# Optimization experiments

Measured on AMD Instinct MI355X. Metric: run time of the kernel, lower is better.

The kernel has to match this reference:

```python
import jax, jax.numpy as jnp
import numpy as np

N_EMBED = 384
NUM_HEADS = 6
HEAD_SIZE = N_EMBED // NUM_HEADS  # 64
B, T = 8, 2048


def setup_inputs() -> dict:
    key = jax.random.key(0)
    ks = jax.random.split(key, 8)
    s = 1.0 / np.sqrt(N_EMBED)
    query = jax.random.normal(ks[0], (B, T, N_EMBED), dtype=jnp.float32)
    key_t = jax.random.normal(ks[1], (B, T, N_EMBED), dtype=jnp.float32)
    value = jax.random.normal(ks[2], (B, T, N_EMBED), dtype=jnp.float32)
    # causal-style mask, broadcastable over (B, H)
    mask = jnp.tril(jnp.ones((T, T), dtype=jnp.int32))[None, None]
    Wk = jax.random.normal(ks[3], (N_EMBED, N_EMBED), dtype=jnp.float32) * s
    Wq = jax.random.normal(ks[4], (N_EMBED, N_EMBED), dtype=jnp.float32) * s
    Wv = jax.random.normal(ks[5], (N_EMBED, N_EMBED), dtype=jnp.float32) * s
    Wproj = jax.random.normal(ks[6], (N_EMBED, N_EMBED), dtype=jnp.float32) * s
    bproj = jnp.zeros((N_EMBED,), dtype=jnp.float32)
    return {"query": query, "key": key_t, "value": value, "mask": mask,
            "Wk": Wk, "Wq": Wq, "Wv": Wv, "Wproj": Wproj, "bproj": bproj}


def _split_heads(x):
    b, t, c = x.shape
    return x.reshape(b, t, NUM_HEADS, c // NUM_HEADS).transpose(0, 2, 1, 3)  # [B,H,T,D]


def reference(query, key, value, mask, Wk, Wq, Wv, Wproj, bproj):
    b, t, c = query.shape
    # NOTE: source swaps names: k = key_proj(query), q = query_proj(key)
    k = _split_heads(query @ Wk.T)
    q = _split_heads(key @ Wq.T)
    v = _split_heads(value @ Wv.T)
    # scale by full C (not head_size), as in the source
    wei = jnp.einsum("bhqd,bhkd->bhqk", q, k) * (c ** -0.5)
    # masked_fill with 0 BEFORE softmax (faithful to source)
    wei = jnp.where(mask == 0, jnp.float32(0.0), wei)
    wei = jax.nn.softmax(wei, axis=-1)
    out = jnp.einsum("bhqk,bhkd->bhqd", wei, v)
    out = out.transpose(0, 2, 1, 3).reshape(b, t, c)
    out = out @ Wproj.T + bproj  # dropout is identity at inference
    return out
```

## Files before the change

### kernel.cpp

```cpp
#include <hip/hip_runtime.h>
#include <hip/hip_bf16.h>


#define TT 2048
#define CC 384
#define HH 6
#define DD 64
#define SCALE 0.05103103630798288f
#define SCALE2 0.07362223f

typedef __bf16 bf16x8 __attribute__((ext_vector_type(8)));
typedef __bf16 bf16x4 __attribute__((ext_vector_type(4)));
typedef float f32x4 __attribute__((ext_vector_type(4)));

__device__ __forceinline__ int swz(int row, int byteInRow) {
    return row * 128 + (byteInRow ^ ((row & 7) << 4));
}

__global__ __launch_bounds__(256) void qkv_proj_kernel(
    const float* __restrict__ query, const float* __restrict__ key,
    const float* __restrict__ value, const float* __restrict__ Wk,
    const float* __restrict__ Wq, const float* __restrict__ Wv,
    __bf16* __restrict__ Kb, __bf16* __restrict__ Qb, __bf16* __restrict__ VTb)
{
    __shared__ __align__(16) char smem[49152];

    const int tid = threadIdx.x;
    const int wid = tid >> 6, lane = tid & 63;
    const int lrow = lane & 15, g = lane >> 4;
    const int pid = blockIdx.z;
    const int m0 = blockIdx.x * 128, n0 = blockIdx.y * 64;
    const float* X = (pid == 0) ? query : ((pid == 1) ? key : value);
    const float* W = (pid == 0) ? Wk : ((pid == 1) ? Wq : Wv);

    const int xrow = tid >> 4, xcol = (tid & 15) * 4;
    const float* xp = X + (size_t)(m0 + xrow) * CC + xcol;
    const float* wp = W + (size_t)(n0 + (tid >> 4)) * CC + xcol;

    f32x4 xr[8], wr[4];

    f32x4 acc[2][4];
#pragma unroll
    for (int i = 0; i < 2; ++i)
#pragma unroll
        for (int j = 0; j < 4; ++j) acc[i][j] = (f32x4){0.f, 0.f, 0.f, 0.f};

#pragma unroll
    for (int i = 0; i < 8; ++i) xr[i] = *(const f32x4*)(xp + (size_t)i * 16 * CC);
#pragma unroll
    for (int i = 0; i < 4; ++i) wr[i] = *(const f32x4*)(wp + (size_t)i * 16 * CC);
    {
        char* Xd = smem;
        char* Wd = smem + 32768;
#pragma unroll
        for (int i = 0; i < 8; ++i) {
            bf16x4 hh;
            hh[0] = (__bf16)xr[i][0]; hh[1] = (__bf16)xr[i][1];
            hh[2] = (__bf16)xr[i][2]; hh[3] = (__bf16)xr[i][3];
            *(bf16x4*)(Xd + swz(xrow + i * 16, xcol * 2)) = hh;
        }
#pragma unroll
        for (int i = 0; i < 4; ++i) {
            bf16x4 hh;
            hh[0] = (__bf16)wr[i][0]; hh[1] = (__bf16)wr[i][1];
            hh[2] = (__bf16)wr[i][2]; hh[3] = (__bf16)wr[i][3];
            *(bf16x4*)(Wd + swz((tid >> 4) + i * 16, xcol * 2)) = hh;
        }
    }
    __syncthreads();

    int cur = 0;
    for (int kk = 0; kk < 6; ++kk) {
        if (kk < 5) {
            const int k0 = (kk + 1) * 64;
#pragma unroll
            for (int i = 0; i < 8; ++i) xr[i] = *(const f32x4*)(xp + (size_t)i * 16 * CC + k0);
#pragma unroll
            for (int i = 0; i < 4; ++i) wr[i] = *(const f32x4*)(wp + (size_t)i * 16 * CC + k0);
        }
        const char* Xs = smem + cur * 16384;
        const char* Ws = smem + 32768 + cur * 8192;

        __builtin_amdgcn_s_setprio(1);
        if (pid < 2) {
#pragma unroll
            for (int kc = 0; kc < 2; ++kc) {
                int kb = kc * 64 + g * 16;
                bf16x8 a0 = *(bf16x8*)(Xs + swz(wid * 32 + lrow, kb));
                bf16x8 a1 = *(bf16x8*)(Xs + swz(wid * 32 + 16 + lrow, kb));
#pragma unroll
                for (int nf = 0; nf < 4; ++nf) {
                    bf16x8 b = *(bf16x8*)(Ws + swz(nf * 16 + lrow, kb));
                    acc[0][nf] = __builtin_amdgcn_mfma_f32_16x16x32_bf16(a0, b, acc[0][nf], 0, 0, 0);
                    acc[1][nf] = __builtin_amdgcn_mfma_f32_16x16x32_bf16(a1, b, acc[1][nf], 0, 0, 0);
                }
            }
        } else {
#pragma unroll
            for (int kc = 0; kc < 2; ++kc) {
                int kb = kc * 64 + g * 16;
                bf16x8 b0 = *(bf16x8*)(Xs + swz(wid * 32 + lrow, kb));
                bf16x8 b1 = *(bf16x8*)(Xs + swz(wid * 32 + 16 + lrow, kb));
#pragma unroll
                for (int nf = 0; nf < 4; ++nf) {
                    bf16x8 a = *(bf16x8*)(Ws + swz(nf * 16 + lrow, kb));
                    acc[0][nf] = __builtin_amdgcn_mfma_f32_16x16x32_bf16(a, b0, acc[0][nf], 0, 0, 0);
                    acc[1][nf] = __builtin_amdgcn_mfma_f32_16x16x32_bf16(a, b1, acc[1][nf], 0, 0, 0);
                }
            }
        }
        __builtin_amdgcn_s_setprio(0);

        if (kk < 5) {
            char* Xd = smem + (cur ^ 1) * 16384;
            char* Wd = smem + 32768 + (cur ^ 1) * 8192;
#pragma unroll
            for (int i = 0; i < 8; ++i) {
                bf16x4 hh;
                hh[0] = (__bf16)xr[i][0]; hh[1] = (__bf16)xr[i][1];
                hh[2] = (__bf16)xr[i][2]; hh[3] = (__bf16)xr[i][3];
                *(bf16x4*)(Xd + swz(xrow + i * 16, xcol * 2)) = hh;
            }
#pragma unroll
            for (int i = 0; i < 4; ++i) {
                bf16x4 hh;
                hh[0] = (__bf16)wr[i][0]; hh[1] = (__bf16)wr[i][1];
                hh[2] = (__bf16)wr[i][2]; hh[3] = (__bf16)wr[i][3];
                *(bf16x4*)(Wd + swz((tid >> 4) + i * 16, xcol * 2)) = hh;
            }
        }
        __syncthreads();
        cur ^= 1;
    }

    if (pid < 2) {
        __bf16* out = (pid == 0) ? Kb : Qb;
#pragma unroll
        for (int mf = 0; mf < 2; ++mf)
#pragma unroll
            for (int nf = 0; nf < 4; ++nf)
#pragma unroll
                for (int r = 0; r < 4; ++r) {
                    int m = m0 + wid * 32 + mf * 16 + g * 4 + r;
                    int n = n0 + nf * 16 + lrow;
                    int b = m >> 11, t = m & 2047, h = n >> 6, d = n & 63;
                    out[((size_t)(b * HH + h) * TT + t) * DD + d] = (__bf16)acc[mf][nf][r];
                }
    } else {
#pragma unroll
        for (int mf = 0; mf < 2; ++mf)
#pragma unroll
            for (int nf = 0; nf < 4; ++nf)
#pragma unroll
                for (int r = 0; r < 4; ++r) {
                    int n = n0 + nf * 16 + g * 4 + r;
                    int m = m0 + wid * 32 + mf * 16 + lrow;
                    int b = m >> 11, t = m & 2047, h = n >> 6, d = n & 63;
                    VTb[((size_t)(b * HH + h) * DD + d) * TT + t] = (__bf16)acc[mf][nf][r];
                }
    }
}

__global__ __launch_bounds__(256) void suffix_kernel(
    const __bf16* __restrict__ VTb, float* __restrict__ Ssuf)
{
    __shared__ float tsum[4][32];
    const int bh = blockIdx.x;
    const int tid = threadIdx.x, wid = tid >> 6, lane = tid & 63;

#pragma unroll
    for (int it = 0; it < 4; ++it) {
        const int dr = blockIdx.y * 16 + wid * 4 + it;
        const __bf16* src = VTb + (size_t)(bh * DD + dr) * TT;
#pragma unroll
        for (int step = 0; step < 4; ++step) {
            bf16x8 v = *(const bf16x8*)(src + step * 512 + lane * 8);
            float sacc = 0.f;
#pragma unroll
            for (int i = 0; i < 8; ++i) sacc += (float)v[i];
            sacc += __shfl_xor(sacc, 1);
            sacc += __shfl_xor(sacc, 2);
            sacc += __shfl_xor(sacc, 4);
            if ((lane & 7) == 0) tsum[wid][step * 8 + (lane >> 3)] = sacc;
        }
        float s2 = 0.f;
        for (int j = 0; j < 32; ++j) {
            float tv = tsum[wid][j];
            if (j >= lane) s2 += tv;
        }
        if (lane <= 32) Ssuf[(size_t)(bh * 33 + lane) * 64 + dr] = s2;
    }
}

__global__ __launch_bounds__(256, 3) void attn_kernel(
    const __bf16* __restrict__ Qb, const __bf16* __restrict__ Kb,
    const __bf16* __restrict__ VTb, const float* __restrict__ Ssuf,
    __bf16* __restrict__ attn)
{
    __shared__ __align__(16) char smem[32768];
    const int tid = threadIdx.x;
    const int wid = tid >> 6, lane = tid & 63;
    const int lrow = lane & 15, g = lane >> 4;

    const int i = blockIdx.x;
    const int xcd = i & 7;
    const int j = i >> 3;
    const int rank = j / 6;
    const int bh = xcd * 6 + (j % 6);
    const int Qt = 15 - rank;
    const int q0 = Qt * 128;
    const int nkt = 2 * Qt + 2;

    const int qloc = wid * 32 + lrow;
    const __bf16* qp = Qb + ((size_t)bh * TT + q0 + qloc) * DD + g * 8;
    bf16x8 qb[2][2];
    qb[0][0] = *(const bf16x8*)(qp);
    qb[0][1] = *(const bf16x8*)(qp + 32);
    qb[1][0] = *(const bf16x8*)(qp + 16 * DD);
    qb[1][1] = *(const bf16x8*)(qp + 16 * DD + 32);

    const int r0 = tid >> 3;
    const int c8 = (tid & 7) * 8;
    const __bf16* kbase = Kb + (size_t)bh * TT * DD;
    const __bf16* vbase = VTb + (size_t)bh * DD * TT;

    bf16x8 kr0, kr1, vr0, vr1;

    f32x4 o[2][4];
#pragma unroll
    for (int mf = 0; mf < 2; ++mf)
#pragma unroll
        for (int ds = 0; ds < 4; ++ds) o[mf][ds] = (f32x4){0.f, 0.f, 0.f, 0.f};
    float z0 = 0.f, z1 = 0.f;

    kr0 = *(const bf16x8*)(kbase + (size_t)r0 * DD + c8);
    kr1 = *(const bf16x8*)(kbase + (size_t)(r0 + 32) * DD + c8);
    vr0 = *(const bf16x8*)(vbase + (size_t)r0 * TT + c8);
    vr1 = *(const bf16x8*)(vbase + (size_t)(r0 + 32) * TT + c8);
    {
        char* Kd = smem;
        char* Vd = smem + 16384;
        *(bf16x8*)(Kd + swz(r0, c8 * 2)) = kr0;
        *(bf16x8*)(Kd + swz(r0 + 32, c8 * 2)) = kr1;
        *(bf16x8*)(Vd + swz(r0, c8 * 2)) = vr0;
        *(bf16x8*)(Vd + swz(r0 + 32, c8 * 2)) = vr1;
    }
    __syncthreads();

    int cur = 0;
    for (int kt = 0; kt < nkt; ++kt) {
        if (kt + 1 < nkt) {
            const int n0 = (kt + 1) * 64;
            kr0 = *(const bf16x8*)(kbase + (size_t)(n0 + r0) * DD + c8);
            kr1 = *(const bf16x8*)(kbase + (size_t)(n0 + r0 + 32) * DD + c8);
            vr0 = *(const bf16x8*)(vbase + (size_t)r0 * TT + n0 + c8);
            vr1 = *(const bf16x8*)(vbase + (size_t)(r0 + 32) * TT + n0 + c8);
        }
        const char* Kc = smem + cur * 8192;
        const char* Vc = smem + 16384 + cur * 8192;
        const bool dm = (kt >= 2 * Qt);

        bf16x8 kfr[2][4];
#pragma unroll
        for (int kc = 0; kc < 2; ++kc)
#pragma unroll
            for (int j16 = 0; j16 < 4; ++j16)
                kfr[kc][j16] = *(const bf16x8*)(Kc + swz(j16 * 16 + lrow, kc * 64 + g * 16));

        f32x4 st[2][4];
#pragma unroll
        for (int mf = 0; mf < 2; ++mf)
#pragma unroll
            for (int j16 = 0; j16 < 4; ++j16) st[mf][j16] = (f32x4){0.f, 0.f, 0.f, 0.f};
        __builtin_amdgcn_s_setprio(1);
#pragma unroll
        for (int kc = 0; kc < 2; ++kc)
#pragma unroll
            for (int mf = 0; mf < 2; ++mf)
#pragma unroll
                for (int j16 = 0; j16 < 4; ++j16)
                    st[mf][j16] = __builtin_amdgcn_mfma_f32_16x16x32_bf16(
                        kfr[kc][j16], qb[mf][kc], st[mf][j16], 0, 0, 0);
        __builtin_amdgcn_s_setprio(0);

        bf16x8 vfr[2][4];
#pragma unroll
        for (int kc = 0; kc < 2; ++kc)
#pragma unroll
            for (int ds = 0; ds < 4; ++ds) {
                union { bf16x8 v8; bf16x4 h[2]; } u;
                u.h[0] = *(const bf16x4*)(Vc + swz(ds * 16 + lrow, kc * 64 + 8 * g));
                u.h[1] = *(const bf16x4*)(Vc + swz(ds * 16 + lrow, kc * 64 + 8 * g + 32));
                vfr[kc][ds] = u.v8;
            }

#pragma unroll
        for (int mf = 0; mf < 2; ++mf) {
            const int qg = q0 + qloc + mf * 16;
            bf16x8 pb0, pb1;
            float zz = 0.f;
#pragma unroll
            for (int j16 = 0; j16 < 4; ++j16) {
#pragma unroll
                for (int r = 0; r < 4; ++r) {
                    float p;
                    if (dm && (kt * 64 + j16 * 16 + g * 4 + r > qg)) p = 1.0f;
                    else p = exp2f(st[mf][j16][r] * SCALE2);
                    zz += p;
                    if (j16 < 2) pb0[(j16 & 1) * 4 + r] = (__bf16)p;
                    else         pb1[(j16 & 1) * 4 + r] = (__bf16)p;
                }
            }
            if (mf == 0) z0 += zz; else z1 += zz;

            __builtin_amdgcn_s_setprio(1);
#pragma unroll
            for (int kc = 0; kc < 2; ++kc) {
                bf16x8 pf = kc ? pb1 : pb0;
#pragma unroll
                for (int ds = 0; ds < 4; ++ds)
                    o[mf][ds] = __builtin_amdgcn_mfma_f32_16x16x32_bf16(
                        vfr[kc][ds], pf, o[mf][ds], 0, 0, 0);
            }
            __builtin_amdgcn_s_setprio(0);
        }

        if (kt + 1 < nkt) {
            char* Kd = smem + (cur ^ 1) * 8192;
            char* Vd = smem + 16384 + (cur ^ 1) * 8192;
            *(bf16x8*)(Kd + swz(r0, c8 * 2)) = kr0;
            *(bf16x8*)(Kd + swz(r0 + 32, c8 * 2)) = kr1;
            *(bf16x8*)(Vd + swz(r0, c8 * 2)) = vr0;
            *(bf16x8*)(Vd + swz(r0 + 32, c8 * 2)) = vr1;
        }
        __syncthreads();
        cur ^= 1;
    }

    const float fut = (float)(TT - nkt * 64);
    z0 += __shfl_xor(z0, 16); z0 += __shfl_xor(z0, 32);
    z1 += __shfl_xor(z1, 16); z1 += __shfl_xor(z1, 32);
    const float inv0 = 1.0f / (z0 + fut);
    const float inv1 = 1.0f / (z1 + fut);

    const float* suf = Ssuf + ((size_t)bh * 33 + nkt) * 64;
    const int b = bh / HH, h = bh % HH;
#pragma unroll
    for (int mf = 0; mf < 2; ++mf) {
        const int t = q0 + qloc + mf * 16;
        const float inv = mf ? inv1 : inv0;
        __bf16* orow = attn + ((size_t)(b * TT + t)) * CC + h * DD;
#pragma unroll
        for (int ds = 0; ds < 4; ++ds) {
            f32x4 sv = *(const f32x4*)(suf + ds * 16 + g * 4);
            bf16x4 w;
#pragma unroll
            for (int r = 0; r < 4; ++r) w[r] = (__bf16)((o[mf][ds][r] + sv[r]) * inv);
            *(bf16x4*)(orow + ds * 16 + g * 4) = w;
        }
    }
}

__global__ __launch_bounds__(256) void out_proj_kernel(
    const __bf16* __restrict__ A, const float* __restrict__ W,
    const float* __restrict__ bias, float* __restrict__ out)
{
    __shared__ __align__(16) char smem[49152];
    const int tid = threadIdx.x;
    const int wid = tid >> 6, lane = tid & 63;
    const int lrow = lane & 15, g = lane >> 4;
    const int m0 = blockIdx.x * 128, n0 = blockIdx.y * 64;

    const int arow = tid >> 3, ac8 = (tid & 7) * 8;
    const __bf16* ap = A + (size_t)(m0 + arow) * CC + ac8;
    const int wrow = tid >> 4, wcol = (tid & 15) * 4;
    const float* wp = W + (size_t)(n0 + wrow) * CC + wcol;

    bf16x8 ar[4];
    f32x4 wr[4];

    f32x4 acc[2][4];
#pragma unroll
    for (int i = 0; i < 2; ++i)
#pragma unroll
        for (int j = 0; j < 4; ++j) acc[i][j] = (f32x4){0.f, 0.f, 0.f, 0.f};

#pragma unroll
    for (int i = 0; i < 4; ++i) ar[i] = *(const bf16x8*)(ap + (size_t)i * 32 * CC);
#pragma unroll
    for (int i = 0; i < 4; ++i) wr[i] = *(const f32x4*)(wp + (size_t)i * 16 * CC);
    {
        char* Ad = smem;
        char* Wd = smem + 32768;
#pragma unroll
        for (int i = 0; i < 4; ++i)
            *(bf16x8*)(Ad + swz(arow + i * 32, ac8 * 2)) = ar[i];
#pragma unroll
        for (int i = 0; i < 4; ++i) {
            bf16x4 hh;
            hh[0] = (__bf16)wr[i][0]; hh[1] = (__bf16)wr[i][1];
            hh[2] = (__bf16)wr[i][2]; hh[3] = (__bf16)wr[i][3];
            *(bf16x4*)(Wd + swz(wrow + i * 16, wcol * 2)) = hh;
        }
    }
    __syncthreads();

    int cur = 0;
    for (int kk = 0; kk < 6; ++kk) {
        if (kk < 5) {
            const int k0 = (kk + 1) * 64;
#pragma unroll
            for (int i = 0; i < 4; ++i) ar[i] = *(const bf16x8*)(ap + (size_t)i * 32 * CC + k0);
#pragma unroll
            for (int i = 0; i < 4; ++i) wr[i] = *(const f32x4*)(wp + (size_t)i * 16 * CC + k0);
        }
        const char* Xs = smem + cur * 16384;
        const char* Ws = smem + 32768 + cur * 8192;

        __builtin_amdgcn_s_setprio(1);
#pragma unroll
        for (int kc = 0; kc < 2; ++kc) {
            int kb = kc * 64 + g * 16;
            bf16x8 a0 = *(bf16x8*)(Xs + swz(wid * 32 + lrow, kb));
            bf16x8 a1 = *(bf16x8*)(Xs + swz(wid * 32 + 16 + lrow, kb));
#pragma unroll
            for (int nf = 0; nf < 4; ++nf) {
                bf16x8 b = *(bf16x8*)(Ws + swz(nf * 16 + lrow, kb));
                acc[0][nf] = __builtin_amdgcn_mfma_f32_16x16x32_bf16(a0, b, acc[0][nf], 0, 0, 0);
                acc[1][nf] = __builtin_amdgcn_mfma_f32_16x16x32_bf16(a1, b, acc[1][nf], 0, 0, 0);
            }
        }
        __builtin_amdgcn_s_setprio(0);

        if (kk < 5) {
            char* Ad = smem + (cur ^ 1) * 16384;
            char* Wd = smem + 32768 + (cur ^ 1) * 8192;
#pragma unroll
            for (int i = 0; i < 4; ++i)
                *(bf16x8*)(Ad + swz(arow + i * 32, ac8 * 2)) = ar[i];
#pragma unroll
            for (int i = 0; i < 4; ++i) {
                bf16x4 hh;
                hh[0] = (__bf16)wr[i][0]; hh[1] = (__bf16)wr[i][1];
                hh[2] = (__bf16)wr[i][2]; hh[3] = (__bf16)wr[i][3];
                *(bf16x4*)(Wd + swz(wrow + i * 16, wcol * 2)) = hh;
            }
        }
        __syncthreads();
        cur ^= 1;
    }

#pragma unroll
    for (int nf = 0; nf < 4; ++nf) {
        float bv = bias[n0 + nf * 16 + lrow];
#pragma unroll
        for (int mf = 0; mf < 2; ++mf)
#pragma unroll
            for (int r = 0; r < 4; ++r) {
                int m = m0 + wid * 32 + mf * 16 + g * 4 + r;
                out[(size_t)m * CC + n0 + nf * 16 + lrow] = acc[mf][nf][r] + bv;
            }
    }
}

extern "C" void kernel_launch(void* const* d_in, const int* in_sizes, int n_in,
                              void* d_out, int out_size, void* d_ws, size_t ws_size,
                              hipStream_t stream)
{
    (void)in_sizes; (void)n_in; (void)out_size; (void)ws_size;
    const float* query = (const float*)d_in[0];
    const float* key   = (const float*)d_in[1];
    const float* value = (const float*)d_in[2];
    const float* Wk    = (const float*)d_in[4];
    const float* Wq    = (const float*)d_in[5];
    const float* Wv    = (const float*)d_in[6];
    const float* Wproj = (const float*)d_in[7];
    const float* bproj = (const float*)d_in[8];
    float* out = (float*)d_out;

    char* ws = (char*)d_ws;
    const size_t SZ = 12582912;
    __bf16* Qb   = (__bf16*)(ws);
    __bf16* Kb   = (__bf16*)(ws + SZ);
    __bf16* VTb  = (__bf16*)(ws + 2 * SZ);
    __bf16* Ab   = (__bf16*)(ws + 3 * SZ);
    float*  Ssuf = (float*)(ws + 4 * SZ);

    qkv_proj_kernel<<<dim3(128, 6, 3), 256, 0, stream>>>(query, key, value,
                                                         Wk, Wq, Wv, Kb, Qb, VTb);
    suffix_kernel<<<dim3(48, 4), 256, 0, stream>>>(VTb, Ssuf);
    attn_kernel<<<dim3(768), 256, 0, stream>>>(Qb, Kb, VTb, Ssuf, Ab);
    out_proj_kernel<<<dim3(128, 6), 256, 0, stream>>>(Ab, Wproj, bproj, out);
}
```

Measured before the change: 263.9 us.

## Fold softmax scale into Q, use MFMA row-sum, specialize masked tiles

The softmax scale is folded into Q when Q is written out in the projection kernel, which removes a multiply per score. exp2f is replaced with the raw hardware exp2 builtin. The row sum is now computed by an extra MFMA against a ones vector instead of scalar adds and cross-lane shuffles. The loop is split so that the diagonal-mask check exists only in the last two tiles, which removes per-element branching elsewhere. The costs are an added MFMA per P chunk, and a Z that is now summed from bf16-rounded P values, which slightly changes the numerics.

Result: faster. 232.7 us (-11.8%).

```diff
diff --git a/kernel.cpp b/kernel.cpp
--- a/kernel.cpp
+++ b/kernel.cpp
@@ -1,13 +1,19 @@
 #include <hip/hip_runtime.h>
 #include <hip/hip_bf16.h>
+#include <type_traits>
 
 
 #define TT 2048
 #define CC 384
 #define HH 6
 #define DD 64
-#define SCALE 0.05103103630798288f
 #define SCALE2 0.07362223f
+
+#if __has_builtin(__builtin_amdgcn_exp2f)
+#define EXP2(x) __builtin_amdgcn_exp2f(x)
+#else
+#define EXP2(x) exp2f(x)
+#endif
 
 typedef __bf16 bf16x8 __attribute__((ext_vector_type(8)));
 typedef __bf16 bf16x4 __attribute__((ext_vector_type(4)));
@@ -135,6 +141,7 @@
 
     if (pid < 2) {
         __bf16* out = (pid == 0) ? Kb : Qb;
+        const float sc = (pid == 1) ? SCALE2 : 1.0f;
 #pragma unroll
         for (int mf = 0; mf < 2; ++mf)
 #pragma unroll
@@ -144,7 +151,7 @@
                     int m = m0 + wid * 32 + mf * 16 + g * 4 + r;
                     int n = n0 + nf * 16 + lrow;
                     int b = m >> 11, t = m & 2047, h = n >> 6, d = n & 63;
-                    out[((size_t)(b * HH + h) * TT + t) * DD + d] = (__bf16)acc[mf][nf][r];
+                    out[((size_t)(b * HH + h) * TT + t) * DD + d] = (__bf16)(acc[mf][nf][r] * sc);
                 }
     } else {
 #pragma unroll
@@ -219,6 +226,10 @@
     qb[1][0] = *(const bf16x8*)(qp + 16 * DD);
     qb[1][1] = *(const bf16x8*)(qp + 16 * DD + 32);
 
+    bf16x8 onesf;
+#pragma unroll
+    for (int ii = 0; ii < 8; ++ii) onesf[ii] = (__bf16)1.0f;
+
     const int r0 = tid >> 3;
     const int c8 = (tid & 7) * 8;
     const __bf16* kbase = Kb + (size_t)bh * TT * DD;
@@ -231,7 +242,9 @@
     for (int mf = 0; mf < 2; ++mf)
 #pragma unroll
         for (int ds = 0; ds < 4; ++ds) o[mf][ds] = (f32x4){0.f, 0.f, 0.f, 0.f};
-    float z0 = 0.f, z1 = 0.f;
+    f32x4 zacc[2];
+    zacc[0] = (f32x4){0.f, 0.f, 0.f, 0.f};
+    zacc[1] = (f32x4){0.f, 0.f, 0.f, 0.f};
 
     kr0 = *(const bf16x8*)(kbase + (size_t)r0 * DD + c8);
     kr1 = *(const bf16x8*)(kbase + (size_t)(r0 + 32) * DD + c8);
@@ -248,7 +261,8 @@
     __syncthreads();
 
     int cur = 0;
-    for (int kt = 0; kt < nkt; ++kt) {
+    auto body = [&](int kt, auto dmc) {
+        constexpr bool DM = decltype(dmc)::value;
         if (kt + 1 < nkt) {
             const int n0 = (kt + 1) * 64;
             kr0 = *(const bf16x8*)(kbase + (size_t)(n0 + r0) * DD + c8);
@@ -258,7 +272,6 @@
         }
         const char* Kc = smem + cur * 8192;
         const char* Vc = smem + 16384 + cur * 8192;
-        const bool dm = (kt >= 2 * Qt);
 
         bf16x8 kfr[2][4];
 #pragma unroll
@@ -298,20 +311,17 @@
         for (int mf = 0; mf < 2; ++mf) {
             const int qg = q0 + qloc + mf * 16;
             bf16x8 pb0, pb1;
-            float zz = 0.f;
 #pragma unroll
             for (int j16 = 0; j16 < 4; ++j16) {
 #pragma unroll
                 for (int r = 0; r < 4; ++r) {
                     float p;
-                    if (dm && (kt * 64 + j16 * 16 + g * 4 + r > qg)) p = 1.0f;
-                    else p = exp2f(st[mf][j16][r] * SCALE2);
-                    zz += p;
+                    if (DM && (kt * 64 + j16 * 16 + g * 4 + r > qg)) p = 1.0f;
+                    else p = EXP2(st[mf][j16][r]);
                     if (j16 < 2) pb0[(j16 & 1) * 4 + r] = (__bf16)p;
                     else         pb1[(j16 & 1) * 4 + r] = (__bf16)p;
                 }
             }
-            if (mf == 0) z0 += zz; else z1 += zz;
 
             __builtin_amdgcn_s_setprio(1);
 #pragma unroll
@@ -321,6 +331,8 @@
                 for (int ds = 0; ds < 4; ++ds)
                     o[mf][ds] = __builtin_amdgcn_mfma_f32_16x16x32_bf16(
                         vfr[kc][ds], pf, o[mf][ds], 0, 0, 0);
+                zacc[mf] = __builtin_amdgcn_mfma_f32_16x16x32_bf16(
+                    onesf, pf, zacc[mf], 0, 0, 0);
             }
             __builtin_amdgcn_s_setprio(0);
         }
@@ -335,13 +347,15 @@
         }
         __syncthreads();
         cur ^= 1;
-    }
+    };
+
+    int kt = 0;
+    for (; kt < nkt - 2; ++kt) body(kt, std::false_type{});
+    for (; kt < nkt; ++kt) body(kt, std::true_type{});
 
     const float fut = (float)(TT - nkt * 64);
-    z0 += __shfl_xor(z0, 16); z0 += __shfl_xor(z0, 32);
-    z1 += __shfl_xor(z1, 16); z1 += __shfl_xor(z1, 32);
-    const float inv0 = 1.0f / (z0 + fut);
-    const float inv1 = 1.0f / (z1 + fut);
+    const float inv0 = 1.0f / (zacc[0][0] + fut);
+    const float inv1 = 1.0f / (zacc[1][0] + fut);
 
     const float* suf = Ssuf + ((size_t)bh * 33 + nkt) * 64;
     const int b = bh / HH, h = bh % HH;
```
